# Kernel optimization log

Measured on AMD Instinct MI355X. Metric: run time of the kernel, lower is better.

Reference implementation:

```python
import jax, jax.numpy as jnp
import numpy as np
import math

B, C, H, W = 16, 256, 128, 128
IC = 32  # inter_channels = in_channels // r


def setup_inputs() -> dict:
    key = jax.random.key(0)
    ks = jax.random.split(key, 7)
    s_in = 1.0 / math.sqrt(C)   # ~ conv kaiming-uniform scale for C->IC 1x1 conv
    s_out = 1.0 / math.sqrt(IC)  # for IC->C 1x1 conv
    return {
        "x": jax.random.normal(ks[0], (B, C, H, W), dtype=jnp.float32),
        "g_w": jax.random.normal(ks[1], (IC, C), dtype=jnp.float32) * s_in,
        "g_b": jax.random.normal(ks[2], (IC,), dtype=jnp.float32) * s_in,
        "theta_w": jax.random.normal(ks[3], (IC, C), dtype=jnp.float32) * s_in,
        "theta_b": jax.random.normal(ks[4], (IC,), dtype=jnp.float32) * s_in,
        "w_w": jax.random.normal(ks[5], (C, IC), dtype=jnp.float32) * s_out,
        "w_b": jax.random.normal(ks[6], (C,), dtype=jnp.float32) * s_out,
    }


def reference(x, g_w, g_b, theta_w, theta_b, w_w, w_b):
    b, c, h, w = x.shape
    m = h * w
    ic = g_w.shape[0]
    xf = x.reshape(b, c, m)  # (B, C, M)
    # 1x1 convs == per-pixel channel matmuls
    g_x = jnp.einsum('ic,bcm->bim', g_w, xf) + g_b[None, :, None]      # (B, IC, M)
    t = jnp.einsum('ic,bcm->bim', theta_w, xf) + theta_b[None, :, None]  # (B, IC, M)
    # sigma = theta_x_T @ I_hat @ theta_x with I_hat = I/M - 11^T/M^2
    #       = (t t^T)/M - mu mu^T  (closed form; avoids (M,M) matrix)
    mu = jnp.mean(t, axis=-1)  # (B, IC)
    sigma = jnp.einsum('bim,bjm->bij', t, t) / m - mu[:, :, None] * mu[:, None, :]
    sigma = sigma / math.sqrt(ic)
    attn = jax.nn.softmax(sigma, axis=-1)  # (B, IC, IC)
    y = jnp.einsum('bij,bjm->bim', attn, g_x)  # (B, IC, M)
    w_y = jnp.einsum('ci,bim->bcm', w_w, y) + w_b[None, :, None]  # (B, C, M)
    return (w_y + xf).reshape(b, c, h, w)
```

## Files before the change

kernel.cpp:

```cpp
#include <hip/hip_runtime.h>
#include <math.h>

constexpr int Bn  = 16;
constexpr int Cn  = 256;
constexpr int Mn  = 16384;
constexpr int ICn = 32;

typedef float v4f   __attribute__((ext_vector_type(4)));
typedef short short8 __attribute__((ext_vector_type(8)));

constexpr size_t OFF_GX  = 0;
constexpr size_t OFF_WBF = OFF_GX  + (size_t)Bn * ICn * Mn;
constexpr size_t OFF_WCT = OFF_WBF + 8192;
constexpr size_t OFF_TT  = OFF_WCT + (size_t)Bn * ICn * Cn;
constexpr size_t OFF_MU  = OFF_TT  + (size_t)Bn * ICn * ICn;

__device__ inline unsigned short f2bf(float f) {
    unsigned u = __float_as_uint(f);
    u += 0x7fffu + ((u >> 16) & 1u);
    return (unsigned short)(u >> 16);
}

__global__ void k0_prep_w(const float* __restrict__ g_w,
                          const float* __restrict__ th_w,
                          unsigned short* __restrict__ wbf) {
    int idx = blockIdx.x * 256 + threadIdx.x;
    int row = idx >> 8, ks = idx & 255;
    int slot = ks >> 3;
    int k = ((slot ^ (row & 7)) << 3) | (ks & 7);
    float v = (row < ICn) ? g_w[row * Cn + k] : th_w[(row - ICn) * Cn + k];
    wbf[idx] = f2bf(v);
}

__global__ __launch_bounds__(256, 4) void k1_mfma(
    const float* __restrict__ x,
    const unsigned short* __restrict__ wbf,
    const float* __restrict__ g_b,
    const float* __restrict__ theta_b,
    float* __restrict__ gx,
    float* __restrict__ tt,
    float* __restrict__ mu)
{
    __shared__ __align__(16) unsigned short Ws[64 * 256];
    __shared__ __align__(16) unsigned short Ts[32 * 72];
    __shared__ float mu_s[ICn];

    const int tx   = threadIdx.x;
    const int b    = blockIdx.y;
    const int m0   = blockIdx.x * 64;
    const int lane = tx & 63;
    const int w    = tx >> 6;
    const int ln15 = lane & 15;
    const int q    = lane >> 4;

    {
        const int4* src = (const int4*)wbf;
        int4* dst = (int4*)Ws;
        #pragma unroll
        for (int i = 0; i < 8; ++i) dst[tx + 256 * i] = src[tx + 256 * i];
    }
    if (tx < ICn) mu_s[tx] = 0.f;
    __syncthreads();

    v4f acc[4];
    #pragma unroll
    for (int nt = 0; nt < 4; ++nt) acc[nt] = (v4f){0.f, 0.f, 0.f, 0.f};

    const float* xbase = x + ((size_t)b * Cn + q * 8) * Mn + m0 + w * 16 + ln15;

    float xf[8];
    #pragma unroll
    for (int j = 0; j < 8; ++j) xf[j] = xbase[(size_t)j * Mn];

    #pragma unroll
    for (int kc = 0; kc < 8; ++kc) {
        short8 a;
        #pragma unroll
        for (int j = 0; j < 8; ++j) a[j] = (short)f2bf(xf[j]);
        if (kc < 7) {
            #pragma unroll
            for (int j = 0; j < 8; ++j)
                xf[j] = xbase[(size_t)((kc + 1) * 32 + j) * Mn];
        }
        #pragma unroll
        for (int nt = 0; nt < 4; ++nt) {
            int row  = nt * 16 + ln15;
            int slot = (kc * 4 + q) ^ (row & 7);
            short8 bf = *(const short8*)&Ws[row * 256 + slot * 8];
            acc[nt] = __builtin_amdgcn_mfma_f32_16x16x32_bf16(a, bf, acc[nt], 0, 0, 0);
        }
    }

    #pragma unroll
    for (int nt = 0; nt < 2; ++nt) {
        int row = nt * 16 + ln15;
        float bb = g_b[row];
        float* gp = gx + ((size_t)b * ICn + row) * Mn + m0 + w * 16 + q * 4;
        #pragma unroll
        for (int r = 0; r < 4; ++r) gp[r] = acc[nt][r] + bb;
    }

    #pragma unroll
    for (int nt = 2; nt < 4; ++nt) {
        int tr = (nt - 2) * 16 + ln15;
        float bb = theta_b[tr];
        float s = 0.f;
        #pragma unroll
        for (int r = 0; r < 4; ++r) {
            float tv = acc[nt][r] + bb;
            Ts[tr * 72 + w * 16 + q * 4 + r] = f2bf(tv);
            s += tv;
        }
        s += __shfl_xor(s, 16);
        s += __shfl_xor(s, 32);
        if (q == 0) atomicAdd(&mu_s[tr], s);
    }
    __syncthreads();

    {
        int i0 = (w & 1) * 16, j0 = (w >> 1) * 16;
        v4f at = (v4f){0.f, 0.f, 0.f, 0.f};
        #pragma unroll
        for (int pc = 0; pc < 2; ++pc) {
            short8 A  = *(const short8*)&Ts[(i0 + ln15) * 72 + pc * 32 + q * 8];
            short8 Bv = *(const short8*)&Ts[(j0 + ln15) * 72 + pc * 32 + q * 8];
            at = __builtin_amdgcn_mfma_f32_16x16x32_bf16(A, Bv, at, 0, 0, 0);
        }
        float* ttb = tt + (size_t)b * ICn * ICn;
        #pragma unroll
        for (int r = 0; r < 4; ++r)
            atomicAdd(&ttb[(i0 + q * 4 + r) * ICn + j0 + ln15], at[r]);
    }
    if (tx < ICn) atomicAdd(&mu[b * ICn + tx], mu_s[tx]);
}

__global__ void k2_attn(const float* __restrict__ tt,
                        const float* __restrict__ mu_in,
                        const float* __restrict__ w_w,
                        float* __restrict__ wct)
{
    __shared__ float s_mu[ICn];
    __shared__ float s_sig[ICn][ICn];
    __shared__ float s_attn[ICn][ICn];
    const int b  = blockIdx.x;
    const int tx = threadIdx.x;

    if (tx < ICn) s_mu[tx] = mu_in[b * ICn + tx] * (1.f / Mn);
    __syncthreads();

    for (int p = tx; p < ICn * ICn; p += 256) {
        int i = p >> 5, j = p & 31;
        s_sig[i][j] = (tt[b * ICn * ICn + p] * (1.f / Mn) - s_mu[i] * s_mu[j])
                      * 0.17677669529663687f;
    }
    __syncthreads();

    if (tx < ICn) {
        float mx = -1e30f;
        #pragma unroll
        for (int j = 0; j < ICn; ++j) mx = fmaxf(mx, s_sig[tx][j]);
        float e[ICn];
        float sum = 0.f;
        #pragma unroll
        for (int j = 0; j < ICn; ++j) { e[j] = __expf(s_sig[tx][j] - mx); sum += e[j]; }
        float r = 1.f / sum;
        #pragma unroll
        for (int j = 0; j < ICn; ++j) s_attn[tx][j] = e[j] * r;
    }
    __syncthreads();

    const int c = tx;
    float wr[ICn];
    #pragma unroll
    for (int i = 0; i < ICn; i += 4) {
        float4 v = *(const float4*)(w_w + c * ICn + i);
        wr[i] = v.x; wr[i + 1] = v.y; wr[i + 2] = v.z; wr[i + 3] = v.w;
    }
    for (int j = 0; j < ICn; ++j) {
        float s = 0.f;
        #pragma unroll
        for (int i = 0; i < ICn; ++i) s += wr[i] * s_attn[i][j];
        wct[((size_t)b * ICn + j) * Cn + c] = s;
    }
}

__global__ __launch_bounds__(256, 4) void k3_out(
    const float* __restrict__ x,
    const float* __restrict__ gx,
    const float* __restrict__ wct,
    const float* __restrict__ w_b,
    float* __restrict__ out)
{
    __shared__ float wc_s[ICn][Cn];
    __shared__ float gx_s[ICn][64];
    __shared__ float wb_s[Cn];

    const int tx = threadIdx.x;
    const int b  = blockIdx.y;
    const int m0 = blockIdx.x * 64;

    {
        const float4* src = (const float4*)(wct + (size_t)b * ICn * Cn);
        float4* dst = (float4*)wc_s;
        #pragma unroll
        for (int p = tx; p < ICn * Cn / 4; p += 256) dst[p] = src[p];
    }
    {
        int r  = tx >> 3;
        int c8 = (tx & 7) * 8;
        const float* g = gx + ((size_t)b * ICn + r) * Mn + m0 + c8;
        *(float4*)&gx_s[r][c8]     = *(const float4*)g;
        *(float4*)&gx_s[r][c8 + 4] = *(const float4*)(g + 4);
    }
    if (tx < 64) ((float4*)wb_s)[tx] = ((const float4*)w_b)[tx];
    __syncthreads();

    const int mg = tx & 15;
    const int cg = tx >> 4;
    float acc[16][4] = {};

    #pragma unroll
    for (int j = 0; j < ICn; ++j) {
        float4 g4 = *(const float4*)&gx_s[j][mg * 4];
        #pragma unroll
        for (int cc = 0; cc < 16; ++cc) {
            float w = wc_s[j][cg * 16 + cc];
            acc[cc][0] += w * g4.x;
            acc[cc][1] += w * g4.y;
            acc[cc][2] += w * g4.z;
            acc[cc][3] += w * g4.w;
        }
    }

    const size_t mbase = (size_t)b * Cn * Mn + m0 + mg * 4;
    #pragma unroll
    for (int cc = 0; cc < 16; ++cc) {
        int c = cg * 16 + cc;
        float4 xv = *(const float4*)(x + mbase + (size_t)c * Mn);
        float wb = wb_s[c];
        float4 o;
        o.x = acc[cc][0] + xv.x + wb;
        o.y = acc[cc][1] + xv.y + wb;
        o.z = acc[cc][2] + xv.z + wb;
        o.w = acc[cc][3] + xv.w + wb;
        *(float4*)(out + mbase + (size_t)c * Mn) = o;
    }
}

extern "C" void kernel_launch(void* const* d_in, const int* in_sizes, int n_in,
                              void* d_out, int out_size, void* d_ws, size_t ws_size,
                              hipStream_t stream) {
    const float* x    = (const float*)d_in[0];
    const float* g_w  = (const float*)d_in[1];
    const float* g_b  = (const float*)d_in[2];
    const float* th_w = (const float*)d_in[3];
    const float* th_b = (const float*)d_in[4];
    const float* w_w  = (const float*)d_in[5];
    const float* w_b  = (const float*)d_in[6];
    float* out = (float*)d_out;
    float* ws  = (float*)d_ws;

    float* gx            = ws + OFF_GX;
    unsigned short* wbf  = (unsigned short*)(ws + OFF_WBF);
    float* wct           = ws + OFF_WCT;
    float* tt            = ws + OFF_TT;
    float* mu            = ws + OFF_MU;

    hipMemsetAsync(tt, 0, (size_t)(Bn * ICn * ICn + Bn * ICn) * sizeof(float), stream);

    k0_prep_w<<<64, 256, 0, stream>>>(g_w, th_w, wbf);
    k1_mfma<<<dim3(Mn / 64, Bn), 256, 0, stream>>>(x, wbf, g_b, th_b, gx, tt, mu);
    k2_attn<<<Bn, 256, 0, stream>>>(tt, mu, w_w, wct);
    k3_out<<<dim3(Mn / 64, Bn), 256, 0, stream>>>(x, gx, wct, w_b, out);
}
```

Before: 562.9 us.

## Fold g-conv, attention and output conv into one per-batch CxC bf16 matrix

The g projection is no longer materialised. Instead, w_w·attn·g_w is folded per batch into a 256x256 bf16 weight image with an effective bias. The output kernel then reads x again and applies this CxC matrix with MFMA, staging the weights in LDS through global_load_lds. This removes the write and read of the B×IC×M gx intermediate and shrinks the stats kernel to the theta projection only. In exchange, the output pass does 8x more MFMA work and uses a large 64KB LDS tile, which lowers occupancy. Rounding the folded weights to bf16 also adds error.

```diff
diff --git a/kernel.cpp b/kernel.cpp
--- a/kernel.cpp
+++ b/kernel.cpp
@@ -6,14 +6,14 @@
 constexpr int Mn  = 16384;
 constexpr int ICn = 32;
 
-typedef float v4f   __attribute__((ext_vector_type(4)));
+typedef float v4f    __attribute__((ext_vector_type(4)));
 typedef short short8 __attribute__((ext_vector_type(8)));
 
-constexpr size_t OFF_GX  = 0;
-constexpr size_t OFF_WBF = OFF_GX  + (size_t)Bn * ICn * Mn;
-constexpr size_t OFF_WCT = OFF_WBF + 8192;
-constexpr size_t OFF_TT  = OFF_WCT + (size_t)Bn * ICn * Cn;
-constexpr size_t OFF_MU  = OFF_TT  + (size_t)Bn * ICn * ICn;
+constexpr size_t OFF_WTH  = 0;
+constexpr size_t OFF_TT   = OFF_WTH + 4096;
+constexpr size_t OFF_MU   = OFF_TT  + (size_t)Bn * ICn * ICn;
+constexpr size_t OFF_BEFF = OFF_MU  + (size_t)Bn * ICn;
+constexpr size_t OFF_WIMG = OFF_BEFF + (size_t)Bn * Cn;
 
 __device__ inline unsigned short f2bf(float f) {
     unsigned u = __float_as_uint(f);
@@ -21,27 +21,30 @@
     return (unsigned short)(u >> 16);
 }
 
-__global__ void k0_prep_w(const float* __restrict__ g_w,
-                          const float* __restrict__ th_w,
+__device__ inline void gload_lds16(const void* g, void* l) {
+    __builtin_amdgcn_global_load_lds(
+        (const __attribute__((address_space(1))) unsigned int*)g,
+        (__attribute__((address_space(3))) unsigned int*)l,
+        16, 0, 0);
+}
+
+__global__ void k0_prep_w(const float* __restrict__ th_w,
                           unsigned short* __restrict__ wbf) {
     int idx = blockIdx.x * 256 + threadIdx.x;
     int row = idx >> 8, ks = idx & 255;
     int slot = ks >> 3;
     int k = ((slot ^ (row & 7)) << 3) | (ks & 7);
-    float v = (row < ICn) ? g_w[row * Cn + k] : th_w[(row - ICn) * Cn + k];
-    wbf[idx] = f2bf(v);
-}
-
-__global__ __launch_bounds__(256, 4) void k1_mfma(
+    wbf[idx] = f2bf(th_w[row * Cn + k]);
+}
+
+__global__ __launch_bounds__(256, 4) void k1_stats(
     const float* __restrict__ x,
     const unsigned short* __restrict__ wbf,
-    const float* __restrict__ g_b,
     const float* __restrict__ theta_b,
-    float* __restrict__ gx,
     float* __restrict__ tt,
     float* __restrict__ mu)
 {
-    __shared__ __align__(16) unsigned short Ws[64 * 256];
+    __shared__ __align__(16) unsigned short Ws[32 * 256];
     __shared__ __align__(16) unsigned short Ts[32 * 72];
     __shared__ float mu_s[ICn];
 
@@ -57,14 +60,14 @@
         const int4* src = (const int4*)wbf;
         int4* dst = (int4*)Ws;
         #pragma unroll
-        for (int i = 0; i < 8; ++i) dst[tx + 256 * i] = src[tx + 256 * i];
+        for (int i = 0; i < 4; ++i) dst[tx + 256 * i] = src[tx + 256 * i];
     }
     if (tx < ICn) mu_s[tx] = 0.f;
     __syncthreads();
 
-    v4f acc[4];
-    #pragma unroll
-    for (int nt = 0; nt < 4; ++nt) acc[nt] = (v4f){0.f, 0.f, 0.f, 0.f};
+    v4f acc[2];
+    #pragma unroll
+    for (int nt = 0; nt < 2; ++nt) acc[nt] = (v4f){0.f, 0.f, 0.f, 0.f};
 
     const float* xbase = x + ((size_t)b * Cn + q * 8) * Mn + m0 + w * 16 + ln15;
 
@@ -83,7 +86,7 @@
                 xf[j] = xbase[(size_t)((kc + 1) * 32 + j) * Mn];
         }
         #pragma unroll
-        for (int nt = 0; nt < 4; ++nt) {
+        for (int nt = 0; nt < 2; ++nt) {
             int row  = nt * 16 + ln15;
             int slot = (kc * 4 + q) ^ (row & 7);
             short8 bf = *(const short8*)&Ws[row * 256 + slot * 8];
@@ -93,16 +96,7 @@
 
     #pragma unroll
     for (int nt = 0; nt < 2; ++nt) {
-        int row = nt * 16 + ln15;
-        float bb = g_b[row];
-        float* gp = gx + ((size_t)b * ICn + row) * Mn + m0 + w * 16 + q * 4;
-        #pragma unroll
-        for (int r = 0; r < 4; ++r) gp[r] = acc[nt][r] + bb;
-    }
-
-    #pragma unroll
-    for (int nt = 2; nt < 4; ++nt) {
-        int tr = (nt - 2) * 16 + ln15;
+        int tr = nt * 16 + ln15;
         float bb = theta_b[tr];
         float s = 0.f;
         #pragma unroll
@@ -134,15 +128,23 @@
     if (tx < ICn) atomicAdd(&mu[b * ICn + tx], mu_s[tx]);
 }
 
-__global__ void k2_attn(const float* __restrict__ tt,
+__global__ void k2_fold(const float* __restrict__ tt,
                         const float* __restrict__ mu_in,
+                        const float* __restrict__ g_w,
+                        const float* __restrict__ g_b,
                         const float* __restrict__ w_w,
-                        float* __restrict__ wct)
+                        const float* __restrict__ w_b,
+                        unsigned short* __restrict__ wimg,
+                        float* __restrict__ beff)
 {
     __shared__ float s_mu[ICn];
     __shared__ float s_sig[ICn][ICn];
-    __shared__ float s_attn[ICn][ICn];
+    __shared__ float s_attn[ICn][ICn + 1];
+    __shared__ float s_gw[ICn][64];
+    __shared__ float s_gb[ICn];
+
     const int b  = blockIdx.x;
+    const int kc = blockIdx.y;
     const int tx = threadIdx.x;
 
     if (tx < ICn) s_mu[tx] = mu_in[b * ICn + tx] * (1.f / Mn);
@@ -153,6 +155,11 @@
         s_sig[i][j] = (tt[b * ICn * ICn + p] * (1.f / Mn) - s_mu[i] * s_mu[j])
                       * 0.17677669529663687f;
     }
+    for (int p = tx; p < ICn * 64; p += 256) {
+        int j = p >> 6, kk = p & 63;
+        s_gw[j][kk] = g_w[j * Cn + kc * 64 + kk];
+    }
+    if (tx < ICn) s_gb[tx] = g_b[tx];
     __syncthreads();
 
     if (tx < ICn) {
@@ -176,74 +183,133 @@
         float4 v = *(const float4*)(w_w + c * ICn + i);
         wr[i] = v.x; wr[i + 1] = v.y; wr[i + 2] = v.z; wr[i + 3] = v.w;
     }
+    float a2[ICn];
+    #pragma unroll
     for (int j = 0; j < ICn; ++j) {
         float s = 0.f;
         #pragma unroll
         for (int i = 0; i < ICn; ++i) s += wr[i] * s_attn[i][j];
-        wct[((size_t)b * ICn + j) * Cn + c] = s;
-    }
-}
-
-__global__ __launch_bounds__(256, 4) void k3_out(
+        a2[j] = s;
+    }
+    unsigned short* wrow = wimg + ((size_t)b * Cn + c) * Cn;
+    for (int kk = 0; kk < 64; ++kk) {
+        int k = kc * 64 + kk;
+        float v = 0.f;
+        #pragma unroll
+        for (int j = 0; j < ICn; ++j) v += a2[j] * s_gw[j][kk];
+        int pos = (((k >> 3) ^ (c & 7)) << 3) | (k & 7);
+        wrow[pos] = f2bf(v);
+    }
+    if (kc == 0) {
+        float s = 0.f;
+        #pragma unroll
+        for (int i = 0; i < ICn; ++i) {
+            float ab = 0.f;
+            #pragma unroll
+            for (int j = 0; j < ICn; ++j) ab += s_attn[i][j] * s_gb[j];
+            s += wr[i] * ab;
+        }
+        beff[b * Cn + c] = s + w_b[c];
+    }
+}
+
+__global__ __launch_bounds__(256, 2) void k3_out(
     const float* __restrict__ x,
-    const float* __restrict__ gx,
-    const float* __restrict__ wct,
-    const float* __restrict__ w_b,
+    const unsigned short* __restrict__ wimg,
+    const float* __restrict__ beff,
     float* __restrict__ out)
 {
-    __shared__ float wc_s[ICn][Cn];
-    __shared__ float gx_s[ICn][64];
-    __shared__ float wb_s[Cn];
-
-    const int tx = threadIdx.x;
-    const int b  = blockIdx.y;
-    const int m0 = blockIdx.x * 64;
-
-    {
-        const float4* src = (const float4*)(wct + (size_t)b * ICn * Cn);
-        float4* dst = (float4*)wc_s;
-        #pragma unroll
-        for (int p = tx; p < ICn * Cn / 4; p += 256) dst[p] = src[p];
-    }
-    {
-        int r  = tx >> 3;
-        int c8 = (tx & 7) * 8;
-        const float* g = gx + ((size_t)b * ICn + r) * Mn + m0 + c8;
-        *(float4*)&gx_s[r][c8]     = *(const float4*)g;
-        *(float4*)&gx_s[r][c8 + 4] = *(const float4*)(g + 4);
-    }
-    if (tx < 64) ((float4*)wb_s)[tx] = ((const float4*)w_b)[tx];
-    __syncthreads();
-
-    const int mg = tx & 15;
-    const int cg = tx >> 4;
-    float acc[16][4] = {};
-
-    #pragma unroll
-    for (int j = 0; j < ICn; ++j) {
-        float4 g4 = *(const float4*)&gx_s[j][mg * 4];
-        #pragma unroll
-        for (int cc = 0; cc < 16; ++cc) {
-            float w = wc_s[j][cg * 16 + cc];
-            acc[cc][0] += w * g4.x;
-            acc[cc][1] += w * g4.y;
-            acc[cc][2] += w * g4.z;
-            acc[cc][3] += w * g4.w;
-        }
-    }
-
-    const size_t mbase = (size_t)b * Cn * Mn + m0 + mg * 4;
-    #pragma unroll
-    for (int cc = 0; cc < 16; ++cc) {
-        int c = cg * 16 + cc;
-        float4 xv = *(const float4*)(x + mbase + (size_t)c * Mn);
-        float wb = wb_s[c];
+    __shared__ __align__(16) unsigned short Ws[128 * 256];
+    __shared__ float bb[Cn];
+
+    const int tx   = threadIdx.x;
+    const int b    = blockIdx.y;
+    const int m0   = blockIdx.x * 64;
+    const int lane = tx & 63;
+    const int w    = tx >> 6;
+    const int ln15 = lane & 15;
+    const int q    = lane >> 4;
+
+    const char* gw0 = (const char*)(wimg + (size_t)b * Cn * Cn);
+
+    #pragma unroll
+    for (int i = 0; i < 16; ++i) {
+        int seg = w * 16 + i;
+        gload_lds16(gw0 + seg * 1024 + lane * 16, (char*)Ws + seg * 1024);
+    }
+    if (tx < 64) ((float4*)bb)[tx] = ((const float4*)(beff + b * Cn))[tx];
+
+    const float* xbase = x + ((size_t)b * Cn + q * 8) * Mn + m0 + w * 16 + ln15;
+    short8 a[8];
+    #pragma unroll
+    for (int kc = 0; kc < 8; ++kc) {
+        float xf[8];
+        #pragma unroll
+        for (int j = 0; j < 8; ++j) xf[j] = xbase[(size_t)(kc * 32 + j) * Mn];
+        #pragma unroll
+        for (int j = 0; j < 8; ++j) a[kc][j] = (short)f2bf(xf[j]);
+    }
+    __syncthreads();
+
+    const size_t obase = (size_t)b * Cn * Mn + m0 + w * 16 + q * 4;
+    v4f acc[8];
+
+    #pragma unroll
+    for (int ct = 0; ct < 8; ++ct) acc[ct] = (v4f){0.f, 0.f, 0.f, 0.f};
+    #pragma unroll
+    for (int kc = 0; kc < 8; ++kc) {
+        #pragma unroll
+        for (int ct = 0; ct < 8; ++ct) {
+            int row  = ct * 16 + ln15;
+            int slot = (kc * 4 + q) ^ (row & 7);
+            short8 bf = *(const short8*)&Ws[row * 256 + slot * 8];
+            acc[ct] = __builtin_amdgcn_mfma_f32_16x16x32_bf16(a[kc], bf, acc[ct], 0, 0, 0);
+        }
+    }
+    __syncthreads();
+
+    #pragma unroll
+    for (int i = 0; i < 16; ++i) {
+        int seg = w * 16 + i;
+        gload_lds16(gw0 + 65536 + seg * 1024 + lane * 16, (char*)Ws + seg * 1024);
+    }
+    #pragma unroll
+    for (int ct = 0; ct < 8; ++ct) {
+        int c = ct * 16 + ln15;
+        float4 xv = *(const float4*)(x + obase + (size_t)c * Mn);
+        float wb = bb[c];
         float4 o;
-        o.x = acc[cc][0] + xv.x + wb;
-        o.y = acc[cc][1] + xv.y + wb;
-        o.z = acc[cc][2] + xv.z + wb;
-        o.w = acc[cc][3] + xv.w + wb;
-        *(float4*)(out + mbase + (size_t)c * Mn) = o;
+        o.x = acc[ct][0] + xv.x + wb;
+        o.y = acc[ct][1] + xv.y + wb;
+        o.z = acc[ct][2] + xv.z + wb;
+        o.w = acc[ct][3] + xv.w + wb;
+        *(float4*)(out + obase + (size_t)c * Mn) = o;
+    }
+    __syncthreads();
+
+    #pragma unroll
+    for (int ct = 0; ct < 8; ++ct) acc[ct] = (v4f){0.f, 0.f, 0.f, 0.f};
+    #pragma unroll
+    for (int kc = 0; kc < 8; ++kc) {
+        #pragma unroll
+        for (int ct = 0; ct < 8; ++ct) {
+            int row  = ct * 16 + ln15;
+            int slot = (kc * 4 + q) ^ (row & 7);
+            short8 bf = *(const short8*)&Ws[row * 256 + slot * 8];
+            acc[ct] = __builtin_amdgcn_mfma_f32_16x16x32_bf16(a[kc], bf, acc[ct], 0, 0, 0);
+        }
+    }
+    #pragma unroll
+    for (int ct = 0; ct < 8; ++ct) {
+        int c = 128 + ct * 16 + ln15;
+        float4 xv = *(const float4*)(x + obase + (size_t)c * Mn);
+        float wb = bb[c];
+        float4 o;
+        o.x = acc[ct][0] + xv.x + wb;
+        o.y = acc[ct][1] + xv.y + wb;
+        o.z = acc[ct][2] + xv.z + wb;
+        o.w = acc[ct][3] + xv.w + wb;
+        *(float4*)(out + obase + (size_t)c * Mn) = o;
     }
 }
 
@@ -260,16 +326,16 @@
     float* out = (float*)d_out;
     float* ws  = (float*)d_ws;
 
-    float* gx            = ws + OFF_GX;
-    unsigned short* wbf  = (unsigned short*)(ws + OFF_WBF);
-    float* wct           = ws + OFF_WCT;
+    unsigned short* wth  = (unsigned short*)(ws + OFF_WTH);
     float* tt            = ws + OFF_TT;
     float* mu            = ws + OFF_MU;
+    float* beff          = ws + OFF_BEFF;
+    unsigned short* wimg = (unsigned short*)(ws + OFF_WIMG);
 
     hipMemsetAsync(tt, 0, (size_t)(Bn * ICn * ICn + Bn * ICn) * sizeof(float), stream);
 
-    k0_prep_w<<<64, 256, 0, stream>>>(g_w, th_w, wbf);
-    k1_mfma<<<dim3(Mn / 64, Bn), 256, 0, stream>>>(x, wbf, g_b, th_b, gx, tt, mu);
-    k2_attn<<<Bn, 256, 0, stream>>>(tt, mu, w_w, wct);
-    k3_out<<<dim3(Mn / 64, Bn), 256, 0, stream>>>(x, gx, wct, w_b, out);
-}
+    k0_prep_w<<<32, 256, 0, stream>>>(th_w, wth);
+    k1_stats<<<dim3(Mn / 64, Bn), 256, 0, stream>>>(x, wth, th_b, tt, mu);
+    k2_fold<<<dim3(Bn, 4), 256, 0, stream>>>(tt, mu, g_w, g_b, w_w, w_b, wimg, beff);
+    k3_out<<<dim3(Mn / 64, Bn), 256, 0, stream>>>(x, wimg, beff, out);
+}
```

Measured after the change: 623.5 us. 10.8% more time.
